# Performance work log

Hardware: AMD Instinct MI355X
Metric: run time of the kernel (lower is better)

The kernel has to match this reference:

```python
import jax, jax.numpy as jnp
import numpy as np

N_HEAD = 16


def setup_inputs() -> dict:
    key = jax.random.key(0)
    k1, k2, k3 = jax.random.split(key, 3)
    B, T, C = 2, 2048, 1024
    x = jax.random.normal(k1, (B, T, C), dtype=jnp.float32)
    w_attn = jax.random.normal(k2, (C, 3 * C), dtype=jnp.float32) * 0.02
    w_proj = jax.random.normal(k3, (C, C), dtype=jnp.float32) * 0.02
    return {"x": x, "w_attn": w_attn, "w_proj": w_proj}


def reference(x, w_attn, w_proj):
    B, T, C = x.shape
    H = N_HEAD
    D = C // H
    qkv = x @ w_attn  # [B, T, 3C]
    q, k, v = jnp.split(qkv, 3, axis=2)
    q = q.reshape(B, T, H, D)
    k = k.reshape(B, T, H, D)
    v = v.reshape(B, T, H, D)
    scale = 1.0 / jnp.sqrt(jnp.asarray(D, dtype=x.dtype))
    # Full T x T score matrix, matching the 'standard_attention' path.
    att = jnp.einsum('bthd,bshd->bhts', q, k) * scale  # [B, H, T, T]
    causal = jnp.tril(jnp.ones((T, T), dtype=bool))
    att = jnp.where(causal[None, None, :, :], att, jnp.asarray(-jnp.inf, dtype=att.dtype))
    att = jax.nn.softmax(att, axis=-1)
    # dropout_p is False (== 0.0) in the original module, so no dropout applied.
    y = jnp.einsum('bhts,bshd->bthd', att, v)  # [B, T, H, D]
    y = y.reshape(B, T, C)
    return y @ w_proj
```

## Files before the change

kernel.cpp:

```cpp
#include <hip/hip_runtime.h>
#include <math.h>

#define BB 2
#define TT 2048
#define HH 16
#define DD 64
#define CC 1024
#define C3 3072

typedef __attribute__((ext_vector_type(8))) short bf16x8;
typedef __attribute__((ext_vector_type(4))) short bf16x4;
typedef __attribute__((ext_vector_type(4))) float f32x4;

__device__ __forceinline__ unsigned short f2bf(float f) {
  union { float f; unsigned u; } v; v.f = f;
  unsigned r = v.u + 0x7fffu + ((v.u >> 16) & 1u);
  return (unsigned short)(r >> 16);
}
__device__ __forceinline__ unsigned short f2bf_up(float f) {
  union { float f; unsigned u; } v; v.f = f;
  return (unsigned short)((v.u + 0x8000u) >> 16);
}

__device__ __forceinline__ void async_cp16(const void* g, void* l) {
  __builtin_amdgcn_global_load_lds(
      (const __attribute__((address_space(1))) void*)g,
      (__attribute__((address_space(3))) void*)l, 16, 0, 0);
}

__global__ __launch_bounds__(256)
void prep(const float* __restrict__ x, const float* __restrict__ w_attn,
          const float* __restrict__ w_proj, unsigned short* __restrict__ xb,
          unsigned short* __restrict__ wat, unsigned short* __restrict__ wpt) {
  __shared__ __align__(16) float Ts[64][68];
  const int bx = blockIdx.x, tid = threadIdx.x;
  if (bx < 1024) {
    int i = bx * 256 + tid;
#pragma unroll
    for (int it = 0; it < 4; ++it, i += 262144) {
      const float4 v = ((const float4*)x)[i];
      bf16x4 o = {(short)f2bf(v.x), (short)f2bf(v.y),
                  (short)f2bf(v.z), (short)f2bf(v.w)};
      ((bf16x4*)xb)[i] = o;
    }
    return;
  }
  const float* W;
  unsigned short* WT;
  int Nd, bound, n0, k0;
  float s;
  if (bx < 1792) {
    const int bid = bx - 1024;
    W = w_attn; WT = wat; Nd = 3072; bound = 1024; s = 0.18033688f;
    n0 = (bid % 48) * 64; k0 = (bid / 48) * 64;
  } else {
    const int bid = bx - 1792;
    W = w_proj; WT = wpt; Nd = 1024; bound = 0; s = 1.0f;
    n0 = (bid % 16) * 64; k0 = (bid / 16) * 64;
  }
  const int rl = tid >> 4, c4 = tid & 15;
#pragma unroll
  for (int it = 0; it < 4; ++it) {
    const int r = it * 16 + rl;
    *(float4*)&Ts[r][c4 * 4] =
        *(const float4*)(W + (size_t)(k0 + r) * Nd + n0 + c4 * 4);
  }
  __syncthreads();
#pragma unroll
  for (int it = 0; it < 4; ++it) {
    const int n = it * 16 + rl;
    const float sc = (n0 + n < bound) ? s : 1.0f;
    bf16x4 o = {(short)f2bf(Ts[c4 * 4 + 0][n] * sc),
                (short)f2bf(Ts[c4 * 4 + 1][n] * sc),
                (short)f2bf(Ts[c4 * 4 + 2][n] * sc),
                (short)f2bf(Ts[c4 * 4 + 3][n] * sc)};
    *(bf16x4*)(WT + (size_t)(n0 + n) * CC + k0 + c4 * 4) = o;
  }
}

template <int MODE, int BM>
__global__ __launch_bounds__(256)
void gemm_bf16(const unsigned short* __restrict__ A,
               const unsigned short* __restrict__ BT,
               void* __restrict__ Cout, unsigned short* __restrict__ Vout,
               int M, int N, int K) {
  constexpr int MT = BM / 32;
  __shared__ __align__(16) unsigned short As[BM * 32];
  __shared__ __align__(16) unsigned short Bs[128 * 32];

  const int tid = threadIdx.x;
  const int w = tid >> 6, lane = tid & 63;
  const int l15 = lane & 15, quad = lane >> 4;
  const int wm = w >> 1, wn = w & 1;

  const int row0 = blockIdx.y * BM, col0 = blockIdx.x * 128;

  const int c0 = tid, c1 = tid + 256;
  const int ar0 = c0 >> 2, ak0 = ((c0 & 3) ^ ((c0 >> 3) & 3)) * 8;
  const int ar1 = c1 >> 2, ak1 = ((c1 & 3) ^ ((c1 >> 3) & 3)) * 8;
  const unsigned short* gA0 = A + (size_t)(row0 + ar0) * K + ak0;
  const unsigned short* gA1 = A + (size_t)(row0 + ar1) * K + ak1;
  const unsigned short* gB0 = BT + (size_t)(col0 + ar0) * K + ak0;
  const unsigned short* gB1 = BT + (size_t)(col0 + ar1) * K + ak1;
  const int lds0 = w * 1024, lds1 = 4096 + w * 1024;

  const int fro = l15 * 64 + 16 * (quad ^ ((l15 >> 1) & 3));
  const char* fA = (const char*)As + wm * (BM * 32) + fro;
  const char* fB = (const char*)Bs + wn * 4096 + fro;

  f32x4 acc[MT][4];
#pragma unroll
  for (int i = 0; i < MT; ++i)
#pragma unroll
    for (int j = 0; j < 4; ++j) acc[i][j] = (f32x4){0.f, 0.f, 0.f, 0.f};

  for (int k0 = 0; k0 < K; k0 += 32) {
    if (k0) __syncthreads();
    async_cp16(gA0 + k0, (char*)As + lds0);
    if (BM == 128) async_cp16(gA1 + k0, (char*)As + lds1);
    async_cp16(gB0 + k0, (char*)Bs + lds0);
    async_cp16(gB1 + k0, (char*)Bs + lds1);
    __syncthreads();

    bf16x8 af[MT], bf[4];
#pragma unroll
    for (int mt = 0; mt < MT; ++mt) af[mt] = *(const bf16x8*)(fA + mt * 1024);
#pragma unroll
    for (int nt = 0; nt < 4; ++nt) bf[nt] = *(const bf16x8*)(fB + nt * 1024);
#pragma unroll
    for (int mt = 0; mt < MT; ++mt)
#pragma unroll
      for (int nt = 0; nt < 4; ++nt)
        acc[mt][nt] = __builtin_amdgcn_mfma_f32_16x16x32_bf16(
            af[mt], bf[nt], acc[mt][nt], 0, 0, 0);
  }

  if (MODE == 2 && col0 >= 2048) {
#pragma unroll
    for (int mt = 0; mt < MT; ++mt) {
      const int rbase = row0 + wm * (BM / 2) + mt * 16 + quad * 4;
      const int bq = rbase >> 11, t0 = rbase & 2047;
#pragma unroll
      for (int nt = 0; nt < 4; ++nt) {
        const int col = col0 + wn * 64 + nt * 16 + l15;
        bf16x4 o = {(short)f2bf(acc[mt][nt][0]), (short)f2bf(acc[mt][nt][1]),
                    (short)f2bf(acc[mt][nt][2]), (short)f2bf(acc[mt][nt][3])};
        *(bf16x4*)(Vout + ((size_t)((bq << 10) + col - 2048) << 11) + t0) = o;
      }
    }
  } else if (MODE >= 1) {
    unsigned short* Cb = (unsigned short*)Cout;
#pragma unroll
    for (int mt = 0; mt < MT; ++mt) {
      const int rbase = row0 + wm * (BM / 2) + mt * 16 + quad * 4;
#pragma unroll
      for (int r = 0; r < 4; ++r) {
        unsigned short* cr = Cb + (size_t)(rbase + r) * N + col0 + wn * 64 + l15;
#pragma unroll
        for (int nt = 0; nt < 4; ++nt) cr[nt * 16] = f2bf(acc[mt][nt][r]);
      }
    }
  } else {
    float* Cf = (float*)Cout;
#pragma unroll
    for (int mt = 0; mt < MT; ++mt) {
      const int rbase = row0 + wm * (BM / 2) + mt * 16 + quad * 4;
#pragma unroll
      for (int r = 0; r < 4; ++r) {
        float* cr = Cf + (size_t)(rbase + r) * N + col0 + wn * 64 + l15;
#pragma unroll
        for (int nt = 0; nt < 4; ++nt) cr[nt * 16] = acc[mt][nt][r];
      }
    }
  }
}

__global__ __launch_bounds__(256)
void attn_mfma(const unsigned short* __restrict__ qkvb,
               const unsigned short* __restrict__ vt,
               unsigned short* __restrict__ y) {
  const int n = blockIdx.x;
  const int bh = (n & 7) + 8 * ((n >> 3) & 3);
  const int qpair = n >> 5;
  const int b = bh >> 4, h = bh & 15;
  const int tid = threadIdx.x;
  const int w = tid >> 6;
  const int lane = tid & 63;
  const int l15 = lane & 15, quad = lane >> 4;

  __shared__ __align__(16) char Kb[2 * 8192];
  __shared__ __align__(16) char Vb[2 * 8192];
  __shared__ __align__(16) unsigned short Ps[64 * 76];
  unsigned short* psw = Ps + w * 16 * 76;

  const int lr = lane >> 3;
  const int lc = lane & 7;
  const int srcoff = ((lc ^ lr) << 4);
  const char* ksrc = (const char*)qkvb + ((size_t)(b * TT) * C3 + 1024 + h * 64) * 2;
  const char* vsrc = (const char*)vt + ((size_t)(b * HH + h) * DD * TT) * 2;

  const int fro = l15 * 128 + ((quad ^ (l15 & 7)) << 4);

  bf16x8 onesf;
#pragma unroll
  for (int jj = 0; jj < 8; ++jj)
    onesf[jj] = (short)(l15 == 0 ? 0x3F80 : 0);

  for (int phase = 0; phase < 2; ++phase) {
    const int qt = phase == 0 ? 31 - qpair : qpair;

    if (phase) __syncthreads();

    const unsigned short* qrow =
        qkvb + (size_t)(b * TT + qt * 64 + w * 16 + l15) * C3 + h * DD;
    bf16x8 qf0 = *(const bf16x8*)(qrow + quad * 8);
    bf16x8 qf1 = *(const bf16x8*)(qrow + 32 + quad * 8);

    f32x4 O[4];
#pragma unroll
    for (int ct = 0; ct < 4; ++ct) O[ct] = (f32x4){0.f, 0.f, 0.f, 0.f};
    f32x4 lacc = (f32x4){0.f, 0.f, 0.f, 0.f};

#pragma unroll
    for (int i = 0; i < 2; ++i) {
      async_cp16(ksrc + (size_t)(w * 16 + i * 8 + lr) * (C3 * 2) + srcoff,
                 Kb + w * 2048 + i * 1024);
      async_cp16(vsrc + (size_t)(w * 16 + i * 8 + lr) * (TT * 2) + srcoff,
                 Vb + w * 2048 + i * 1024);
    }

    for (int j = 0; j <= qt; ++j) {
      const int cur = j & 1;
      __syncthreads();

      if (j < qt) {
        const int key1 = (j + 1) * 64;
        char* kd = Kb + (cur ^ 1) * 8192 + w * 2048;
        char* vd = Vb + (cur ^ 1) * 8192 + w * 2048;
#pragma unroll
        for (int i = 0; i < 2; ++i) {
          async_cp16(
              ksrc + (size_t)(key1 + w * 16 + i * 8 + lr) * (C3 * 2) + srcoff,
              kd + i * 1024);
          async_cp16(
              vsrc + (size_t)(w * 16 + i * 8 + lr) * (TT * 2) + key1 * 2 + srcoff,
              vd + i * 1024);
        }
      }

      const char* Kc = Kb + cur * 8192;
      const char* Vc = Vb + cur * 8192;

      f32x4 S[4];
#pragma unroll
      for (int ct = 0; ct < 4; ++ct) {
        bf16x8 k0 = *(const bf16x8*)(Kc + ct * 2048 + fro);
        bf16x8 k1 = *(const bf16x8*)(Kc + ct * 2048 + (fro ^ 64));
        f32x4 z = (f32x4){-12.f, -12.f, -12.f, -12.f};
        z = __builtin_amdgcn_mfma_f32_16x16x32_bf16(qf0, k0, z, 0, 0, 0);
        z = __builtin_amdgcn_mfma_f32_16x16x32_bf16(qf1, k1, z, 0, 0, 0);
        S[ct] = z;
      }

      if (j == qt) {
#pragma unroll
        for (int ct = 0; ct < 4; ++ct)
#pragma unroll
          for (int r = 0; r < 4; ++r)
            if (16 * ct + l15 > w * 16 + quad * 4 + r) S[ct][r] = -INFINITY;
      }

#pragma unroll
      for (int ct = 0; ct < 4; ++ct)
#pragma unroll
        for (int r = 0; r < 4; ++r)
          psw[(quad * 4 + r) * 76 + 16 * ct + l15] = f2bf_up(exp2f(S[ct][r]));

      bf16x8 pf[2];
#pragma unroll
      for (int kh = 0; kh < 2; ++kh) {
        const unsigned short* pr = psw + l15 * 76 + kh * 32 + quad * 8;
        bf16x4 lo = *(const bf16x4*)(pr);
        bf16x4 hi = *(const bf16x4*)(pr + 4);
        bf16x8 f;
#pragma unroll
        for (int jj = 0; jj < 4; ++jj) { f[jj] = lo[jj]; f[4 + jj] = hi[jj]; }
        pf[kh] = f;
      }

      lacc = __builtin_amdgcn_mfma_f32_16x16x32_bf16(pf[0], onesf, lacc, 0, 0, 0);
      lacc = __builtin_amdgcn_mfma_f32_16x16x32_bf16(pf[1], onesf, lacc, 0, 0, 0);
#pragma unroll
      for (int ct = 0; ct < 4; ++ct) {
        bf16x8 v0 = *(const bf16x8*)(Vc + ct * 2048 + fro);
        bf16x8 v1 = *(const bf16x8*)(Vc + ct * 2048 + (fro ^ 64));
        O[ct] = __builtin_amdgcn_mfma_f32_16x16x32_bf16(pf[0], v0, O[ct], 0, 0, 0);
        O[ct] = __builtin_amdgcn_mfma_f32_16x16x32_bf16(pf[1], v1, O[ct], 0, 0, 0);
      }
    }

    float inv[4];
#pragma unroll
    for (int r = 0; r < 4; ++r)
      inv[r] = 1.0f / __shfl(lacc[r], lane & 48, 64);

    unsigned short* yr =
        y + (size_t)(b * TT + qt * 64 + w * 16 + quad * 4) * CC + h * DD + l15;
#pragma unroll
    for (int r = 0; r < 4; ++r)
#pragma unroll
      for (int ct = 0; ct < 4; ++ct)
        yr[(size_t)r * CC + 16 * ct] = f2bf(O[ct][r] * inv[r]);
  }
}

extern "C" void kernel_launch(void* const* d_in, const int* in_sizes, int n_in,
                              void* d_out, int out_size, void* d_ws,
                              size_t ws_size, hipStream_t stream) {
  const float* x      = (const float*)d_in[0];
  const float* w_attn = (const float*)d_in[1];
  const float* w_proj = (const float*)d_in[2];
  float* out = (float*)d_out;

  unsigned short* xb   = (unsigned short*)d_ws;
  unsigned short* wat  = xb + (size_t)4096 * 1024;
  unsigned short* wpt  = wat + (size_t)3072 * 1024;
  unsigned short* qkvb = wpt + (size_t)1024 * 1024;
  unsigned short* vt   = qkvb + (size_t)4096 * 3072;
  unsigned short* yb   = vt + (size_t)BB * HH * DD * TT;

  dim3 blk(256);

  prep<<<2048, blk, 0, stream>>>(x, w_attn, w_proj, xb, wat, wpt);

  gemm_bf16<2, 128><<<dim3(C3 / 128, (BB * TT) / 128), blk, 0, stream>>>(
      xb, wat, qkvb, vt, BB * TT, C3, CC);

  attn_mfma<<<dim3(512, 1, 1), blk, 0, stream>>>(qkvb, vt, yb);

  gemm_bf16<0, 64><<<dim3(CC / 128, (BB * TT) / 64), blk, 0, stream>>>(
      yb, wpt, out, nullptr, BB * TT, CC, CC);
}
```

Baseline: 189.8 us.

## Double-buffer GEMM LDS tiles and transpose attention MFMA operands for packed P stores

The GEMM kernel now uses two LDS buffers so the async global-to-LDS copy of the next K tile is issued before computing on the current one, overlapping loads with MFMA work at the cost of double the shared memory. In attention, MFMA operand order is swapped so scores come out transposed, letting each lane pack four bf16 P values into one 8-byte LDS store and read back whole 16-byte fragments. The all-ones row-sum operand yields the normalizer directly per lane, removing the shuffle, and output stores become 4-wide vector writes. The risk is higher LDS use lowering occupancy, plus correctness depending on the transposed layout and mask being consistent.

After: 192.0 us. Within noise of the previous version (+1.2%).

```diff
diff --git a/kernel.cpp b/kernel.cpp
--- a/kernel.cpp
+++ b/kernel.cpp
@@ -11,6 +11,7 @@
 typedef __attribute__((ext_vector_type(8))) short bf16x8;
 typedef __attribute__((ext_vector_type(4))) short bf16x4;
 typedef __attribute__((ext_vector_type(4))) float f32x4;
+typedef __attribute__((ext_vector_type(2))) unsigned int u32x2;
 
 __device__ __forceinline__ unsigned short f2bf(float f) {
   union { float f; unsigned u; } v; v.f = f;
@@ -85,8 +86,9 @@
                void* __restrict__ Cout, unsigned short* __restrict__ Vout,
                int M, int N, int K) {
   constexpr int MT = BM / 32;
-  __shared__ __align__(16) unsigned short As[BM * 32];
-  __shared__ __align__(16) unsigned short Bs[128 * 32];
+  constexpr int ABYTES = BM * 64;
+  __shared__ __align__(16) unsigned short As[2 * BM * 32];
+  __shared__ __align__(16) unsigned short Bs[2 * 128 * 32];
 
   const int tid = threadIdx.x;
   const int w = tid >> 6, lane = tid & 63;
@@ -105,8 +107,6 @@
   const int lds0 = w * 1024, lds1 = 4096 + w * 1024;
 
   const int fro = l15 * 64 + 16 * (quad ^ ((l15 >> 1) & 3));
-  const char* fA = (const char*)As + wm * (BM * 32) + fro;
-  const char* fB = (const char*)Bs + wn * 4096 + fro;
 
   f32x4 acc[MT][4];
 #pragma unroll
@@ -114,25 +114,39 @@
 #pragma unroll
     for (int j = 0; j < 4; ++j) acc[i][j] = (f32x4){0.f, 0.f, 0.f, 0.f};
 
-  for (int k0 = 0; k0 < K; k0 += 32) {
-    if (k0) __syncthreads();
-    async_cp16(gA0 + k0, (char*)As + lds0);
-    if (BM == 128) async_cp16(gA1 + k0, (char*)As + lds1);
-    async_cp16(gB0 + k0, (char*)Bs + lds0);
-    async_cp16(gB1 + k0, (char*)Bs + lds1);
+  const int nt = K / 32;
+  async_cp16(gA0, (char*)As + lds0);
+  if (BM == 128) async_cp16(gA1, (char*)As + lds1);
+  async_cp16(gB0, (char*)Bs + lds0);
+  async_cp16(gB1, (char*)Bs + lds1);
+
+  for (int i = 0; i < nt; ++i) {
+    const int cur = i & 1;
     __syncthreads();
 
+    if (i + 1 < nt) {
+      const int k1 = (i + 1) * 32;
+      const int alt = cur ^ 1;
+      async_cp16(gA0 + k1, (char*)As + alt * ABYTES + lds0);
+      if (BM == 128) async_cp16(gA1 + k1, (char*)As + alt * ABYTES + lds1);
+      async_cp16(gB0 + k1, (char*)Bs + alt * 8192 + lds0);
+      async_cp16(gB1 + k1, (char*)Bs + alt * 8192 + lds1);
+    }
+
+    const char* fA = (const char*)As + cur * ABYTES + wm * (BM * 32) + fro;
+    const char* fB = (const char*)Bs + cur * 8192 + wn * 4096 + fro;
+
     bf16x8 af[MT], bf[4];
 #pragma unroll
     for (int mt = 0; mt < MT; ++mt) af[mt] = *(const bf16x8*)(fA + mt * 1024);
 #pragma unroll
-    for (int nt = 0; nt < 4; ++nt) bf[nt] = *(const bf16x8*)(fB + nt * 1024);
+    for (int nt2 = 0; nt2 < 4; ++nt2) bf[nt2] = *(const bf16x8*)(fB + nt2 * 1024);
 #pragma unroll
     for (int mt = 0; mt < MT; ++mt)
 #pragma unroll
-      for (int nt = 0; nt < 4; ++nt)
-        acc[mt][nt] = __builtin_amdgcn_mfma_f32_16x16x32_bf16(
-            af[mt], bf[nt], acc[mt][nt], 0, 0, 0);
+      for (int nt2 = 0; nt2 < 4; ++nt2)
+        acc[mt][nt2] = __builtin_amdgcn_mfma_f32_16x16x32_bf16(
+            af[mt], bf[nt2], acc[mt][nt2], 0, 0, 0);
   }
 
   if (MODE == 2 && col0 >= 2048) {
@@ -141,10 +155,10 @@
       const int rbase = row0 + wm * (BM / 2) + mt * 16 + quad * 4;
       const int bq = rbase >> 11, t0 = rbase & 2047;
 #pragma unroll
-      for (int nt = 0; nt < 4; ++nt) {
-        const int col = col0 + wn * 64 + nt * 16 + l15;
-        bf16x4 o = {(short)f2bf(acc[mt][nt][0]), (short)f2bf(acc[mt][nt][1]),
-                    (short)f2bf(acc[mt][nt][2]), (short)f2bf(acc[mt][nt][3])};
+      for (int nt2 = 0; nt2 < 4; ++nt2) {
+        const int col = col0 + wn * 64 + nt2 * 16 + l15;
+        bf16x4 o = {(short)f2bf(acc[mt][nt2][0]), (short)f2bf(acc[mt][nt2][1]),
+                    (short)f2bf(acc[mt][nt2][2]), (short)f2bf(acc[mt][nt2][3])};
         *(bf16x4*)(Vout + ((size_t)((bq << 10) + col - 2048) << 11) + t0) = o;
       }
     }
@@ -157,7 +171,7 @@
       for (int r = 0; r < 4; ++r) {
         unsigned short* cr = Cb + (size_t)(rbase + r) * N + col0 + wn * 64 + l15;
 #pragma unroll
-        for (int nt = 0; nt < 4; ++nt) cr[nt * 16] = f2bf(acc[mt][nt][r]);
+        for (int nt2 = 0; nt2 < 4; ++nt2) cr[nt2 * 16] = f2bf(acc[mt][nt2][r]);
       }
     }
   } else {
@@ -169,7 +183,7 @@
       for (int r = 0; r < 4; ++r) {
         float* cr = Cf + (size_t)(rbase + r) * N + col0 + wn * 64 + l15;
 #pragma unroll
-        for (int nt = 0; nt < 4; ++nt) cr[nt * 16] = acc[mt][nt][r];
+        for (int nt2 = 0; nt2 < 4; ++nt2) cr[nt2 * 16] = acc[mt][nt2][r];
       }
     }
   }
@@ -190,8 +204,8 @@
 
   __shared__ __align__(16) char Kb[2 * 8192];
   __shared__ __align__(16) char Vb[2 * 8192];
-  __shared__ __align__(16) unsigned short Ps[64 * 76];
-  unsigned short* psw = Ps + w * 16 * 76;
+  __shared__ __align__(16) unsigned short Ps[4 * 16 * 72];
+  unsigned short* psw = Ps + w * 16 * 72;
 
   const int lr = lane >> 3;
   const int lc = lane & 7;
@@ -203,8 +217,7 @@
 
   bf16x8 onesf;
 #pragma unroll
-  for (int jj = 0; jj < 8; ++jj)
-    onesf[jj] = (short)(l15 == 0 ? 0x3F80 : 0);
+  for (int jj = 0; jj < 8; ++jj) onesf[jj] = (short)0x3F80;
 
   for (int phase = 0; phase < 2; ++phase) {
     const int qt = phase == 0 ? 31 - qpair : qpair;
@@ -218,7 +231,7 @@
 
     f32x4 O[4];
 #pragma unroll
-    for (int ct = 0; ct < 4; ++ct) O[ct] = (f32x4){0.f, 0.f, 0.f, 0.f};
+    for (int dt = 0; dt < 4; ++dt) O[dt] = (f32x4){0.f, 0.f, 0.f, 0.f};
     f32x4 lacc = (f32x4){0.f, 0.f, 0.f, 0.f};
 
 #pragma unroll
@@ -257,8 +270,8 @@
         bf16x8 k0 = *(const bf16x8*)(Kc + ct * 2048 + fro);
         bf16x8 k1 = *(const bf16x8*)(Kc + ct * 2048 + (fro ^ 64));
         f32x4 z = (f32x4){-12.f, -12.f, -12.f, -12.f};
-        z = __builtin_amdgcn_mfma_f32_16x16x32_bf16(qf0, k0, z, 0, 0, 0);
-        z = __builtin_amdgcn_mfma_f32_16x16x32_bf16(qf1, k1, z, 0, 0, 0);
+        z = __builtin_amdgcn_mfma_f32_16x16x32_bf16(k0, qf0, z, 0, 0, 0);
+        z = __builtin_amdgcn_mfma_f32_16x16x32_bf16(k1, qf1, z, 0, 0, 0);
         S[ct] = z;
       }
 
@@ -267,50 +280,44 @@
         for (int ct = 0; ct < 4; ++ct)
 #pragma unroll
           for (int r = 0; r < 4; ++r)
-            if (16 * ct + l15 > w * 16 + quad * 4 + r) S[ct][r] = -INFINITY;
-      }
-
-#pragma unroll
-      for (int ct = 0; ct < 4; ++ct)
-#pragma unroll
-        for (int r = 0; r < 4; ++r)
-          psw[(quad * 4 + r) * 76 + 16 * ct + l15] = f2bf_up(exp2f(S[ct][r]));
-
-      bf16x8 pf[2];
-#pragma unroll
-      for (int kh = 0; kh < 2; ++kh) {
-        const unsigned short* pr = psw + l15 * 76 + kh * 32 + quad * 8;
-        bf16x4 lo = *(const bf16x4*)(pr);
-        bf16x4 hi = *(const bf16x4*)(pr + 4);
-        bf16x8 f;
-#pragma unroll
-        for (int jj = 0; jj < 4; ++jj) { f[jj] = lo[jj]; f[4 + jj] = hi[jj]; }
-        pf[kh] = f;
-      }
-
-      lacc = __builtin_amdgcn_mfma_f32_16x16x32_bf16(pf[0], onesf, lacc, 0, 0, 0);
-      lacc = __builtin_amdgcn_mfma_f32_16x16x32_bf16(pf[1], onesf, lacc, 0, 0, 0);
+            if (16 * ct + quad * 4 + r > w * 16 + l15) S[ct][r] = -INFINITY;
+      }
+
 #pragma unroll
       for (int ct = 0; ct < 4; ++ct) {
-        bf16x8 v0 = *(const bf16x8*)(Vc + ct * 2048 + fro);
-        bf16x8 v1 = *(const bf16x8*)(Vc + ct * 2048 + (fro ^ 64));
-        O[ct] = __builtin_amdgcn_mfma_f32_16x16x32_bf16(pf[0], v0, O[ct], 0, 0, 0);
-        O[ct] = __builtin_amdgcn_mfma_f32_16x16x32_bf16(pf[1], v1, O[ct], 0, 0, 0);
-      }
-    }
-
-    float inv[4];
-#pragma unroll
-    for (int r = 0; r < 4; ++r)
-      inv[r] = 1.0f / __shfl(lacc[r], lane & 48, 64);
-
+        const unsigned p0 = f2bf_up(exp2f(S[ct][0]));
+        const unsigned p1 = f2bf_up(exp2f(S[ct][1]));
+        const unsigned p2 = f2bf_up(exp2f(S[ct][2]));
+        const unsigned p3 = f2bf_up(exp2f(S[ct][3]));
+        u32x2 d;
+        d[0] = p0 | (p1 << 16);
+        d[1] = p2 | (p3 << 16);
+        *(u32x2*)((char*)psw + l15 * 144 + ct * 32 + quad * 8) = d;
+      }
+
+      bf16x8 pf0 = *(const bf16x8*)((char*)psw + l15 * 144 + quad * 16);
+      bf16x8 pf1 = *(const bf16x8*)((char*)psw + l15 * 144 + 64 + quad * 16);
+
+      lacc = __builtin_amdgcn_mfma_f32_16x16x32_bf16(onesf, pf0, lacc, 0, 0, 0);
+      lacc = __builtin_amdgcn_mfma_f32_16x16x32_bf16(onesf, pf1, lacc, 0, 0, 0);
+#pragma unroll
+      for (int dt = 0; dt < 4; ++dt) {
+        bf16x8 v0 = *(const bf16x8*)(Vc + dt * 2048 + fro);
+        bf16x8 v1 = *(const bf16x8*)(Vc + dt * 2048 + (fro ^ 64));
+        O[dt] = __builtin_amdgcn_mfma_f32_16x16x32_bf16(v0, pf0, O[dt], 0, 0, 0);
+        O[dt] = __builtin_amdgcn_mfma_f32_16x16x32_bf16(v1, pf1, O[dt], 0, 0, 0);
+      }
+    }
+
+    const float inv = 1.0f / lacc[0];
     unsigned short* yr =
-        y + (size_t)(b * TT + qt * 64 + w * 16 + quad * 4) * CC + h * DD + l15;
-#pragma unroll
-    for (int r = 0; r < 4; ++r)
-#pragma unroll
-      for (int ct = 0; ct < 4; ++ct)
-        yr[(size_t)r * CC + 16 * ct] = f2bf(O[ct][r] * inv[r]);
+        y + (size_t)(b * TT + qt * 64 + w * 16 + l15) * CC + h * DD + quad * 4;
+#pragma unroll
+    for (int dt = 0; dt < 4; ++dt) {
+      bf16x4 o = {(short)f2bf(O[dt][0] * inv), (short)f2bf(O[dt][1] * inv),
+                  (short)f2bf(O[dt][2] * inv), (short)f2bf(O[dt][3] * inv)};
+      *(bf16x4*)(yr + dt * 16) = o;
+    }
   }
 }
 
```
